# Kernel optimization log

Measured on AMD Instinct MI355X. Metric: run time of the kernel, lower is better.

The kernel has to match this reference:

```python
import jax, jax.numpy as jnp
import numpy as np

D_MODEL = 1024
NUM_HEADS = 16
DEPTH = D_MODEL // NUM_HEADS
NEG = -1e30


def setup_inputs() -> dict:
    key = jax.random.key(0)
    ks = jax.random.split(key, 12)
    B, S = 4, 2048
    scale = 1.0 / np.sqrt(D_MODEL)
    inp = {
        "v": jax.random.normal(ks[0], (B, S, D_MODEL), dtype=jnp.float32),
        "k": jax.random.normal(ks[1], (B, S, D_MODEL), dtype=jnp.float32),
        "q": jax.random.normal(ks[2], (B, S, D_MODEL), dtype=jnp.float32),
        "mask": jax.random.randint(ks[3], (B, 1, 1, S), 0, 2, dtype=jnp.int32),
        "wq": jax.random.normal(ks[4], (D_MODEL, D_MODEL), dtype=jnp.float32) * scale,
        "bq": jnp.zeros((D_MODEL,), dtype=jnp.float32),
        "wk": jax.random.normal(ks[5], (D_MODEL, D_MODEL), dtype=jnp.float32) * scale,
        "bk": jnp.zeros((D_MODEL,), dtype=jnp.float32),
        "wv": jax.random.normal(ks[6], (D_MODEL, D_MODEL), dtype=jnp.float32) * scale,
        "bv": jnp.zeros((D_MODEL,), dtype=jnp.float32),
        "wo": jax.random.normal(ks[7], (D_MODEL, D_MODEL), dtype=jnp.float32) * scale,
        "bo": jnp.zeros((D_MODEL,), dtype=jnp.float32),
    }
    return inp


def _split_heads(x):
    # [B, S, D] -> [B, H, S, depth]
    B, S, _ = x.shape
    return x.reshape(B, S, NUM_HEADS, DEPTH).transpose(0, 2, 1, 3)


def reference(v, k, q, mask, wq, bq, wk, bk, wv, bv, wo, bo):
    B, Sq, _ = q.shape
    qh = _split_heads(q @ wq + bq)  # [B,H,Sq,depth]
    kh = _split_heads(k @ wk + bk)  # [B,H,Sk,depth]
    vh = _split_heads(v @ wv + bv)  # [B,H,Sk,depth]
    scale = 1.0 / jnp.sqrt(jnp.float32(DEPTH))
    scores = scale * jnp.einsum("bhqd,bhkd->bhqk", qh, kh)
    scores = scores + mask.astype(scores.dtype) * NEG
    attn = jax.nn.softmax(scores, axis=-1)
    out = jnp.einsum("bhqk,bhkd->bhqd", attn, vh)
    out = out.transpose(0, 2, 1, 3).reshape(B, Sq, D_MODEL)
    return out @ wo + bo
```

## Files before the change

kernel.cpp:

```cpp
#include <hip/hip_runtime.h>

typedef _Float16 half_t;
typedef __attribute__((ext_vector_type(8))) _Float16 half8;
typedef __attribute__((ext_vector_type(4))) _Float16 half4;
typedef __attribute__((ext_vector_type(4))) float f32x4;

#define SEQ   2048
#define DM    1024
#define NH    16
#define DEPTH 64

__device__ __forceinline__ void gload16(const void* g, void* l) {
    __builtin_amdgcn_global_load_lds(
        (const __attribute__((address_space(1))) void*)g,
        (__attribute__((address_space(3))) void*)l, 16, 0, 0);
}

__global__ __launch_bounds__(256) void wm_k(
    const float* __restrict__ w0, const float* __restrict__ w1,
    const float* __restrict__ w2, const float* __restrict__ w3,
    half_t* __restrict__ out,
    const int* __restrict__ mask, int* __restrict__ idx, int* __restrict__ cnt)
{
    const int z = blockIdx.z;
    if (z == 4) {
        if (blockIdx.x || blockIdx.y) return;
        const int tid = threadIdx.y * 32 + threadIdx.x;
        const int b = tid >> 6;
        const int lane = tid & 63;
        const int* m = mask + b*SEQ;
        int* ib = idx + b*SEQ;
        int off = 0;
        for (int c = 0; c < SEQ; c += 64) {
            int keep = (m[c + lane] == 0);
            unsigned long long bal = __ballot(keep);
            int pre = __popcll(bal & ((1ull << lane) - 1ull));
            if (keep) ib[off + pre] = c + lane;
            off += __popcll(bal);
        }
        if (lane == 0) cnt[b] = off;
        return;
    }
    __shared__ float tile[32][33];
    const float* srcs[4] = {w0, w1, w2, w3};
    const float* src = srcs[z];
    half_t* dst = out + (size_t)z * DM * DM;
    int n0 = blockIdx.x * 32, k0 = blockIdx.y * 32;
    int tx = threadIdx.x, ty = threadIdx.y;
#pragma unroll
    for (int i = 0; i < 4; ++i)
        tile[ty + 8*i][tx] = src[(size_t)(k0 + ty + 8*i)*DM + n0 + tx];
    __syncthreads();
#pragma unroll
    for (int i = 0; i < 4; ++i)
        dst[(size_t)(n0 + ty + 8*i)*DM + k0 + tx] = (half_t)tile[tx][ty + 8*i];
}

__global__ __launch_bounds__(256) void cvt3_k(
    const float* __restrict__ qsrc, const float* __restrict__ ksrc,
    const float* __restrict__ vsrc,
    const int* __restrict__ idx, const int* __restrict__ cnt,
    half_t* __restrict__ qdst, half_t* __restrict__ kdst, half_t* __restrict__ vdst)
{
    const int bid = blockIdx.x;
    const int t = threadIdx.x;
    if (bid < 4096) {
        size_t i = ((size_t)bid * 256 + t) * 8;
        float4 a = *(const float4*)(qsrc + i);
        float4 b = *(const float4*)(qsrc + i + 4);
        half8 h;
        h[0]=(half_t)a.x; h[1]=(half_t)a.y; h[2]=(half_t)a.z; h[3]=(half_t)a.w;
        h[4]=(half_t)b.x; h[5]=(half_t)b.y; h[6]=(half_t)b.z; h[7]=(half_t)b.w;
        *(half8*)(qdst + i) = h;
        return;
    }
    const int which = (bid >= 4608);
    const float* src = which ? vsrc : ksrc;
    half_t*      dst = which ? vdst : kdst;
    const int r0 = (bid - (which ? 4608 : 4096)) * 16;
    const int b  = r0 >> 11;
    const int nc = cnt[b];
    const int row = r0 + (t >> 4);
    const int jl  = row & (SEQ - 1);
    if (jl >= nc) return;
    const float* sp = src + (size_t)((b << 11) + idx[(b << 11) + jl]) * DM;
    half_t* dp = dst + (size_t)row * DM;
#pragma unroll
    for (int i = 0; i < 8; ++i) {
        int c = i*128 + (t & 15)*8;
        float4 lo = *(const float4*)(sp + c);
        float4 hi = *(const float4*)(sp + c + 4);
        half8 h;
        h[0]=(half_t)lo.x; h[1]=(half_t)lo.y; h[2]=(half_t)lo.z; h[3]=(half_t)lo.w;
        h[4]=(half_t)hi.x; h[5]=(half_t)hi.y; h[6]=(half_t)hi.z; h[7]=(half_t)hi.w;
        *(half8*)(dp + c) = h;
    }
}

__global__ __launch_bounds__(512, 2) void qk8_k(
    const half_t* __restrict__ Aq, const half_t* __restrict__ Ak,
    const half_t* __restrict__ wT,
    const float* __restrict__ bq, const float* __restrict__ bk,
    float qscale,
    half_t* __restrict__ Qh, half_t* __restrict__ Kc)
{
    __shared__ __align__(16) half_t smem[3 * 24576];
    const int flat = blockIdx.x;
    const int wg   = (flat & 7) * 64 + (flat >> 3);
    const int z    = wg >> 8;
    const int rem  = wg & 255;
    const int n0   = (rem & 3) * 256;
    const int m0   = (rem >> 2) * 128;

    const half_t* A    = z ? Ak : Aq;
    const half_t* Bt   = wT + (size_t)z * DM * DM;
    const float*  bias = z ? bk : bq;
    half_t*       Cp   = z ? Kc : Qh;
    const float   os   = z ? 1.0f : qscale;

    const int t = threadIdx.x, lane = t & 63, wave = t >> 6;
    const int wr = wave >> 2, wc = wave & 3;
    const int lr = lane & 15, lq = lane >> 4;

    f32x4 acc[4][4] = {};

#pragma unroll
    for (int kt = 0; kt < 2; ++kt) {
#pragma unroll
        for (int i = 0; i < 2; ++i) {
            int c = i*512 + t;
            gload16(A + (size_t)(m0 + (c>>3))*DM + kt*64 + (c&7)*8,
                    smem + kt*24576 + c*8);
        }
#pragma unroll
        for (int i = 0; i < 4; ++i) {
            int c = i*512 + t;
            gload16(Bt + (size_t)(n0 + (c>>3))*DM + kt*64 + (c&7)*8,
                    smem + kt*24576 + 8192 + c*8);
        }
    }
    asm volatile("s_waitcnt vmcnt(6)" ::: "memory");
    __builtin_amdgcn_s_barrier();

    for (int kt = 0; kt < 16; ++kt) {
        const int cur = kt % 3;
        const half_t* lA = smem + cur*24576;
        const half_t* lB = smem + cur*24576 + 8192;

        half8 af[4][2], bf[4][2];
#pragma unroll
        for (int mi = 0; mi < 4; ++mi)
#pragma unroll
            for (int kk = 0; kk < 2; ++kk)
                af[mi][kk] = *(const half8*)(lA + (wr*64 + mi*16 + lr)*64 + kk*32 + lq*8);
#pragma unroll
        for (int ni = 0; ni < 4; ++ni)
#pragma unroll
            for (int kk = 0; kk < 2; ++kk)
                bf[ni][kk] = *(const half8*)(lB + (wc*64 + ni*16 + lr)*64 + kk*32 + lq*8);

        if (kt + 2 < 16) {
            const int nxt = (kt + 2) % 3;
            const int kn = kt + 2;
#pragma unroll
            for (int i = 0; i < 2; ++i) {
                int c = i*512 + t;
                gload16(A + (size_t)(m0 + (c>>3))*DM + kn*64 + (c&7)*8,
                        smem + nxt*24576 + c*8);
            }
#pragma unroll
            for (int i = 0; i < 4; ++i) {
                int c = i*512 + t;
                gload16(Bt + (size_t)(n0 + (c>>3))*DM + kn*64 + (c&7)*8,
                        smem + nxt*24576 + 8192 + c*8);
            }
        }

        __builtin_amdgcn_s_setprio(1);
#pragma unroll
        for (int mi = 0; mi < 4; ++mi)
#pragma unroll
            for (int ni = 0; ni < 4; ++ni)
#pragma unroll
                for (int kk = 0; kk < 2; ++kk)
                    acc[mi][ni] = __builtin_amdgcn_mfma_f32_16x16x32_f16(af[mi][kk], bf[ni][kk], acc[mi][ni], 0, 0, 0);
        __builtin_amdgcn_s_setprio(0);

        if (kt < 15) {
            if (kt < 14) asm volatile("s_waitcnt vmcnt(6)" ::: "memory");
            else         asm volatile("s_waitcnt vmcnt(0)" ::: "memory");
            __builtin_amdgcn_s_barrier();
        }
    }

#pragma unroll
    for (int mi = 0; mi < 4; ++mi) {
#pragma unroll
        for (int ni = 0; ni < 4; ++ni) {
            int col = n0 + wc*64 + ni*16 + lr;
            float bv = bias[col];
#pragma unroll
            for (int j = 0; j < 4; ++j) {
                int row = m0 + wr*64 + mi*16 + lq*4 + j;
                Cp[(size_t)row*DM + col] = (half_t)((acc[mi][ni][j] + bv) * os);
            }
        }
    }
}

template<bool OUT_F32, bool VEPI>
__global__ __launch_bounds__(512, 2) void proj8_f16(
    const half_t* __restrict__ A, const half_t* __restrict__ Bt,
    const float* __restrict__ bias, float oscale, void* __restrict__ Cp)
{
    __shared__ __align__(16) half_t smem[3 * 24576];
    const int flat = blockIdx.x;
    const int wg   = (flat & 7) * 32 + (flat >> 3);
    const int n0   = (wg & 3) * 256;
    const int m0   = (wg >> 2) * 128;
    const int t = threadIdx.x, lane = t & 63, wave = t >> 6;
    const int wr = wave >> 2, wc = wave & 3;
    const int lr = lane & 15, lq = lane >> 4;

    f32x4 acc[4][4] = {};

#pragma unroll
    for (int kt = 0; kt < 2; ++kt) {
#pragma unroll
        for (int i = 0; i < 2; ++i) {
            int c = i*512 + t;
            gload16(A + (size_t)(m0 + (c>>3))*DM + kt*64 + (c&7)*8,
                    smem + kt*24576 + c*8);
        }
#pragma unroll
        for (int i = 0; i < 4; ++i) {
            int c = i*512 + t;
            gload16(Bt + (size_t)(n0 + (c>>3))*DM + kt*64 + (c&7)*8,
                    smem + kt*24576 + 8192 + c*8);
        }
    }
    asm volatile("s_waitcnt vmcnt(6)" ::: "memory");
    __builtin_amdgcn_s_barrier();

    for (int kt = 0; kt < 16; ++kt) {
        const int cur = kt % 3;
        const half_t* lA = smem + cur*24576;
        const half_t* lB = smem + cur*24576 + 8192;

        half8 af[4][2], bf[4][2];
#pragma unroll
        for (int mi = 0; mi < 4; ++mi)
#pragma unroll
            for (int kk = 0; kk < 2; ++kk)
                af[mi][kk] = *(const half8*)(lA + (wr*64 + mi*16 + lr)*64 + kk*32 + lq*8);
#pragma unroll
        for (int ni = 0; ni < 4; ++ni)
#pragma unroll
            for (int kk = 0; kk < 2; ++kk)
                bf[ni][kk] = *(const half8*)(lB + (wc*64 + ni*16 + lr)*64 + kk*32 + lq*8);

        if (kt + 2 < 16) {
            const int nxt = (kt + 2) % 3;
            const int kn = kt + 2;
#pragma unroll
            for (int i = 0; i < 2; ++i) {
                int c = i*512 + t;
                gload16(A + (size_t)(m0 + (c>>3))*DM + kn*64 + (c&7)*8,
                        smem + nxt*24576 + c*8);
            }
#pragma unroll
            for (int i = 0; i < 4; ++i) {
                int c = i*512 + t;
                gload16(Bt + (size_t)(n0 + (c>>3))*DM + kn*64 + (c&7)*8,
                        smem + nxt*24576 + 8192 + c*8);
            }
        }

        __builtin_amdgcn_s_setprio(1);
#pragma unroll
        for (int mi = 0; mi < 4; ++mi)
#pragma unroll
            for (int ni = 0; ni < 4; ++ni)
#pragma unroll
                for (int kk = 0; kk < 2; ++kk)
                    acc[mi][ni] = __builtin_amdgcn_mfma_f32_16x16x32_f16(af[mi][kk], bf[ni][kk], acc[mi][ni], 0, 0, 0);
        __builtin_amdgcn_s_setprio(0);

        if (kt < 15) {
            if (kt < 14) asm volatile("s_waitcnt vmcnt(6)" ::: "memory");
            else         asm volatile("s_waitcnt vmcnt(0)" ::: "memory");
            __builtin_amdgcn_s_barrier();
        }
    }

    const int b = m0 >> 11;
#pragma unroll
    for (int mi = 0; mi < 4; ++mi) {
#pragma unroll
        for (int ni = 0; ni < 4; ++ni) {
            int col = n0 + wc*64 + ni*16 + lr;
            float bv = bias[col];
            if (VEPI) {
                int rl = (m0 + wr*64 + mi*16 + lq*4) & (SEQ-1);
                int pos = (rl & ~63) | (((rl>>5)&1)<<5) | (((rl>>2)&3)<<3) | (((rl>>4)&1)<<2);
                half4 hv;
#pragma unroll
                for (int j = 0; j < 4; ++j)
                    hv[j] = (half_t)(acc[mi][ni][j] + bv);
                *(half4*)((half_t*)Cp + ((size_t)(b*NH*DEPTH + col))*SEQ + pos) = hv;
            } else {
#pragma unroll
                for (int j = 0; j < 4; ++j) {
                    int row = m0 + wr*64 + mi*16 + lq*4 + j;
                    float vv = (acc[mi][ni][j] + bv) * oscale;
                    if (OUT_F32)
                        ((float*)Cp)[(size_t)row*DM + col] = vv;
                    else
                        ((half_t*)Cp)[(size_t)row*DM + col] = (half_t)vv;
                }
            }
        }
    }
}

__global__ __launch_bounds__(512, 4) void attn_k(
    const half_t* __restrict__ Qh, const half_t* __restrict__ Kc,
    const half_t* __restrict__ Vt, const int* __restrict__ cnt,
    half_t* __restrict__ Oh)
{
    constexpr int KP = 72;
    constexpr int VP = 136;
    __shared__ __align__(16) half_t lK[2][128 * KP];
    __shared__ __align__(16) half_t lV[2][64 * VP];
    const int t = threadIdx.x;
    const int lane = t & 63, wave = t >> 6;
    const int lr = lane & 15, lq = lane >> 4;
    const int flat = blockIdx.x;
    const int rest = flat >> 3;
    const int qb = rest & 7;
    const int bh = (flat & 7) + 8 * (rest >> 3);
    const int b = bh >> 4, h = bh & 15;
    const int q0 = qb * 256;

    const int nc = cnt[b];
    const int ntk = (nc + 127) >> 7;

    const size_t qbase = ((size_t)(b*SEQ + q0 + wave*32 + lr))*DM + h*DEPTH;
    const half8 aq00 = *(const half8*)(Qh + qbase + lq*8);
    const half8 aq01 = *(const half8*)(Qh + qbase + 32 + lq*8);
    const half8 aq10 = *(const half8*)(Qh + qbase + (size_t)16*DM + lq*8);
    const half8 aq11 = *(const half8*)(Qh + qbase + (size_t)16*DM + 32 + lq*8);

    const int krow = t >> 2, kcol = (t & 3) * 16;
    const int vd   = t >> 3, vs   = (t & 7) * 16;
    const half_t* gK = Kc + (size_t)(b*SEQ + krow)*DM + h*DEPTH + kcol;
    const half_t* gV = Vt + ((size_t)bh*DEPTH + vd)*SEQ + vs;

    f32x4 o[2][4] = {};
    f32x4 ol[2] = {};
    half8 onesv;
#pragma unroll
    for (int e = 0; e < 8; ++e) onesv[e] = (half_t)1.0f;
    const f32x4 minit = {-8.0f, -8.0f, -8.0f, -8.0f};

    half8 kr0 = *(const half8*)gK,       kr1 = *(const half8*)(gK + 8);
    half8 vr0 = *(const half8*)gV,       vr1 = *(const half8*)(gV + 8);
    *(half8*)&lK[0][krow*KP + kcol]     = kr0;
    *(half8*)&lK[0][krow*KP + kcol + 8] = kr1;
    *(half8*)&lV[0][vd*VP + vs]         = vr0;
    *(half8*)&lV[0][vd*VP + vs + 8]     = vr1;
    __syncthreads();

    for (int it = 0; it < ntk; ++it) {
        const int cur = it & 1;
        const int kt = it * 128;
        const bool more = (it + 1 < ntk);
        if (more) {
            const half_t* nk = gK + (size_t)(it+1)*128*DM;
            const half_t* nv = gV + (it+1)*128;
            kr0 = *(const half8*)nk;  kr1 = *(const half8*)(nk + 8);
            vr0 = *(const half8*)nv;  vr1 = *(const half8*)(nv + 8);
        }
        const bool full = (kt + 128 <= nc);

#pragma unroll
        for (int c = 0; c < 4; ++c) {
            f32x4 s[2][2] = {{minit, minit}, {minit, minit}};
            __builtin_amdgcn_s_setprio(1);
#pragma unroll
            for (int cc = 0; cc < 2; ++cc) {
                const half_t* kb = &lK[cur][((2*c+cc)*16 + lr)*KP];
                half8 kf0 = *(const half8*)(kb + lq*8);
                half8 kf1 = *(const half8*)(kb + 32 + lq*8);
                s[0][cc] = __builtin_amdgcn_mfma_f32_16x16x32_f16(kf0, aq00, s[0][cc], 0, 0, 0);
                s[0][cc] = __builtin_amdgcn_mfma_f32_16x16x32_f16(kf1, aq01, s[0][cc], 0, 0, 0);
                s[1][cc] = __builtin_amdgcn_mfma_f32_16x16x32_f16(kf0, aq10, s[1][cc], 0, 0, 0);
                s[1][cc] = __builtin_amdgcn_mfma_f32_16x16x32_f16(kf1, aq11, s[1][cc], 0, 0, 0);
            }
            __builtin_amdgcn_s_setprio(0);

            half8 pk0, pk1;
            if (full) {
#pragma unroll
                for (int cc = 0; cc < 2; ++cc)
#pragma unroll
                    for (int r = 0; r < 4; ++r) {
                        pk0[cc*4 + r] = (half_t)__builtin_amdgcn_exp2f(s[0][cc][r]);
                        pk1[cc*4 + r] = (half_t)__builtin_amdgcn_exp2f(s[1][cc][r]);
                    }
            } else {
#pragma unroll
                for (int cc = 0; cc < 2; ++cc)
#pragma unroll
                    for (int r = 0; r < 4; ++r) {
                        float am = (kt + (2*c+cc)*16 + lq*4 + r < nc) ? 0.0f : -1e30f;
                        pk0[cc*4 + r] = (half_t)__builtin_amdgcn_exp2f(s[0][cc][r] + am);
                        pk1[cc*4 + r] = (half_t)__builtin_amdgcn_exp2f(s[1][cc][r] + am);
                    }
            }

            __builtin_amdgcn_s_setprio(1);
#pragma unroll
            for (int ni = 0; ni < 4; ++ni) {
                half8 av = *(const half8*)(&lV[cur][(ni*16 + lr)*VP + c*32 + lq*8]);
                o[0][ni] = __builtin_amdgcn_mfma_f32_16x16x32_f16(av, pk0, o[0][ni], 0, 0, 0);
                o[1][ni] = __builtin_amdgcn_mfma_f32_16x16x32_f16(av, pk1, o[1][ni], 0, 0, 0);
            }
            ol[0] = __builtin_amdgcn_mfma_f32_16x16x32_f16(onesv, pk0, ol[0], 0, 0, 0);
            ol[1] = __builtin_amdgcn_mfma_f32_16x16x32_f16(onesv, pk1, ol[1], 0, 0, 0);
            __builtin_amdgcn_s_setprio(0);
        }

        if (more) {
            *(half8*)&lK[cur^1][krow*KP + kcol]     = kr0;
            *(half8*)&lK[cur^1][krow*KP + kcol + 8] = kr1;
            *(half8*)&lV[cur^1][vd*VP + vs]         = vr0;
            *(half8*)&lV[cur^1][vd*VP + vs + 8]     = vr1;
        }
        __syncthreads();
    }

    half_t* pb = ((half_t*)lK) + wave * 32 * KP;
    float rl0 = 1.0f / ol[0][0];
    float rl1 = 1.0f / ol[1][0];
#pragma unroll
    for (int ni = 0; ni < 4; ++ni)
#pragma unroll
        for (int j = 0; j < 4; ++j) {
            pb[lr*KP + ni*16 + lq*4 + j]        = (half_t)(o[0][ni][j] * rl0);
            pb[(16 + lr)*KP + ni*16 + lq*4 + j] = (half_t)(o[1][ni][j] * rl1);
        }
    __syncthreads();
#pragma unroll
    for (int rr = 0; rr < 4; ++rr) {
        int qq = rr*8 + (lane >> 3);
        int c = (lane & 7) * 8;
        half8 hv = *(const half8*)(pb + qq*KP + c);
        *(half8*)(Oh + (size_t)(b*SEQ + q0 + wave*32 + qq)*DM + h*DEPTH + c) = hv;
    }
}

extern "C" void kernel_launch(void* const* d_in, const int* in_sizes, int n_in,
                              void* d_out, int out_size, void* d_ws, size_t ws_size,
                              hipStream_t stream) {
    (void)in_sizes; (void)n_in; (void)out_size; (void)ws_size;
    const float* v    = (const float*)d_in[0];
    const float* k    = (const float*)d_in[1];
    const float* q    = (const float*)d_in[2];
    const int*   mask = (const int*)  d_in[3];
    const float* wq   = (const float*)d_in[4];
    const float* bq   = (const float*)d_in[5];
    const float* wk   = (const float*)d_in[6];
    const float* bk   = (const float*)d_in[7];
    const float* wv   = (const float*)d_in[8];
    const float* bv   = (const float*)d_in[9];
    const float* wo   = (const float*)d_in[10];
    const float* bo   = (const float*)d_in[11];

    half_t* wT  = (half_t*)d_ws;
    half_t* xfq = wT + 4ull*1024*1024;
    half_t* xfk = xfq + 8ull*1024*1024;
    half_t* xfv = xfk + 8ull*1024*1024;
    half_t* Kc  = xfv + 8ull*1024*1024;
    half_t* Qh  = (half_t*)d_out;
    half_t* Vt  = xfq;
    half_t* O16 = xfv;

    int* idx = (int*)((char*)d_out + 32ull*1024*1024 - 65536);
    int* cnt = idx + 4*SEQ;

    const float qscale = 0.125f * 1.44269504088896340736f;

    wm_k<<<dim3(32,32,5), dim3(32,8), 0, stream>>>(wq, wk, wv, wo, wT, mask, idx, cnt);
    cvt3_k<<<5120, 256, 0, stream>>>(q, k, v, idx, cnt, xfq, xfk, xfv);

    qk8_k<<<512, 512, 0, stream>>>(xfq, xfk, wT, bq, bk, qscale, Qh, Kc);
    proj8_f16<false,true><<<256, 512, 0, stream>>>(xfv, wT + 2ull*1024*1024, bv, 1.0f, Vt);

    attn_k<<<512, 512, 0, stream>>>(Qh, Kc, Vt, cnt, O16);
    proj8_f16<true,false><<<256, 512, 0, stream>>>(O16, wT + 3ull*1024*1024, bo, 1.0f, (float*)d_out);
}
```

Measured before the change: 187.8 us.

## Halve GEMM K-tile to 32 with XOR-swizzled LDS layout in projection kernels

Reduces the K-step of the Q/K and output projection GEMMs from 64 to 32, halving LDS per stage from 144KB to 72KB across three buffers, and doubling the number of pipeline iterations. The global-to-LDS loads now XOR-swizzle the 16-byte chunks by row group, and the fragment reads apply the matching swizzle to avoid LDS bank conflicts. The smaller footprint may allow more workgroups per CU. The cost is twice as many barriers and waitcnt points per tile, with less MFMA work between syncs.

```diff
diff --git a/kernel.cpp b/kernel.cpp
--- a/kernel.cpp
+++ b/kernel.cpp
@@ -97,6 +97,7 @@
     }
 }
 
+
 __global__ __launch_bounds__(512, 2) void qk8_k(
     const half_t* __restrict__ Aq, const half_t* __restrict__ Ak,
     const half_t* __restrict__ wT,
@@ -104,7 +105,7 @@
     float qscale,
     half_t* __restrict__ Qh, half_t* __restrict__ Kc)
 {
-    __shared__ __align__(16) half_t smem[3 * 24576];
+    __shared__ __align__(16) half_t smem[3 * 12288];
     const int flat = blockIdx.x;
     const int wg   = (flat & 7) * 64 + (flat >> 3);
     const int z    = wg >> 8;
@@ -121,58 +122,48 @@
     const int t = threadIdx.x, lane = t & 63, wave = t >> 6;
     const int wr = wave >> 2, wc = wave & 3;
     const int lr = lane & 15, lq = lane >> 4;
-
+    const int lx = (lr >> 2) & 3;
+
+    const int ar = t >> 2,  asl = t & 3;
     f32x4 acc[4][4] = {};
 
 #pragma unroll
     for (int kt = 0; kt < 2; ++kt) {
+        gload16(A + (size_t)(m0 + ar)*DM + kt*32 + ((asl ^ ((ar>>2)&3))*8),
+                smem + kt*12288 + t*8);
 #pragma unroll
         for (int i = 0; i < 2; ++i) {
-            int c = i*512 + t;
-            gload16(A + (size_t)(m0 + (c>>3))*DM + kt*64 + (c&7)*8,
-                    smem + kt*24576 + c*8);
-        }
-#pragma unroll
-        for (int i = 0; i < 4; ++i) {
-            int c = i*512 + t;
-            gload16(Bt + (size_t)(n0 + (c>>3))*DM + kt*64 + (c&7)*8,
-                    smem + kt*24576 + 8192 + c*8);
-        }
-    }
-    asm volatile("s_waitcnt vmcnt(6)" ::: "memory");
+            int c = i*512 + t, r = c>>2, s = c&3;
+            gload16(Bt + (size_t)(n0 + r)*DM + kt*32 + ((s ^ ((r>>2)&3))*8),
+                    smem + kt*12288 + 4096 + c*8);
+        }
+    }
+    asm volatile("s_waitcnt vmcnt(3)" ::: "memory");
     __builtin_amdgcn_s_barrier();
 
-    for (int kt = 0; kt < 16; ++kt) {
+    for (int kt = 0; kt < 32; ++kt) {
         const int cur = kt % 3;
-        const half_t* lA = smem + cur*24576;
-        const half_t* lB = smem + cur*24576 + 8192;
-
-        half8 af[4][2], bf[4][2];
+        const half_t* lA = smem + cur*12288;
+        const half_t* lB = smem + cur*12288 + 4096;
+
+        half8 af[4], bf[4];
 #pragma unroll
         for (int mi = 0; mi < 4; ++mi)
-#pragma unroll
-            for (int kk = 0; kk < 2; ++kk)
-                af[mi][kk] = *(const half8*)(lA + (wr*64 + mi*16 + lr)*64 + kk*32 + lq*8);
+            af[mi] = *(const half8*)(lA + (wr*64 + mi*16 + lr)*32 + ((lq ^ lx))*8);
 #pragma unroll
         for (int ni = 0; ni < 4; ++ni)
-#pragma unroll
-            for (int kk = 0; kk < 2; ++kk)
-                bf[ni][kk] = *(const half8*)(lB + (wc*64 + ni*16 + lr)*64 + kk*32 + lq*8);
-
-        if (kt + 2 < 16) {
+            bf[ni] = *(const half8*)(lB + (wc*64 + ni*16 + lr)*32 + ((lq ^ lx))*8);
+
+        if (kt + 2 < 32) {
             const int nxt = (kt + 2) % 3;
             const int kn = kt + 2;
+            gload16(A + (size_t)(m0 + ar)*DM + kn*32 + ((asl ^ ((ar>>2)&3))*8),
+                    smem + nxt*12288 + t*8);
 #pragma unroll
             for (int i = 0; i < 2; ++i) {
-                int c = i*512 + t;
-                gload16(A + (size_t)(m0 + (c>>3))*DM + kn*64 + (c&7)*8,
-                        smem + nxt*24576 + c*8);
-            }
-#pragma unroll
-            for (int i = 0; i < 4; ++i) {
-                int c = i*512 + t;
-                gload16(Bt + (size_t)(n0 + (c>>3))*DM + kn*64 + (c&7)*8,
-                        smem + nxt*24576 + 8192 + c*8);
+                int c = i*512 + t, r = c>>2, s = c&3;
+                gload16(Bt + (size_t)(n0 + r)*DM + kn*32 + ((s ^ ((r>>2)&3))*8),
+                        smem + nxt*12288 + 4096 + c*8);
             }
         }
 
@@ -181,13 +172,11 @@
         for (int mi = 0; mi < 4; ++mi)
 #pragma unroll
             for (int ni = 0; ni < 4; ++ni)
-#pragma unroll
-                for (int kk = 0; kk < 2; ++kk)
-                    acc[mi][ni] = __builtin_amdgcn_mfma_f32_16x16x32_f16(af[mi][kk], bf[ni][kk], acc[mi][ni], 0, 0, 0);
+                acc[mi][ni] = __builtin_amdgcn_mfma_f32_16x16x32_f16(af[mi], bf[ni], acc[mi][ni], 0, 0, 0);
         __builtin_amdgcn_s_setprio(0);
 
-        if (kt < 15) {
-            if (kt < 14) asm volatile("s_waitcnt vmcnt(6)" ::: "memory");
+        if (kt < 31) {
+            if (kt < 30) asm volatile("s_waitcnt vmcnt(3)" ::: "memory");
             else         asm volatile("s_waitcnt vmcnt(0)" ::: "memory");
             __builtin_amdgcn_s_barrier();
         }
@@ -213,7 +202,7 @@
     const half_t* __restrict__ A, const half_t* __restrict__ Bt,
     const float* __restrict__ bias, float oscale, void* __restrict__ Cp)
 {
-    __shared__ __align__(16) half_t smem[3 * 24576];
+    __shared__ __align__(16) half_t smem[3 * 12288];
     const int flat = blockIdx.x;
     const int wg   = (flat & 7) * 32 + (flat >> 3);
     const int n0   = (wg & 3) * 256;
@@ -221,58 +210,48 @@
     const int t = threadIdx.x, lane = t & 63, wave = t >> 6;
     const int wr = wave >> 2, wc = wave & 3;
     const int lr = lane & 15, lq = lane >> 4;
+    const int lx = (lr >> 2) & 3;
+    const int ar = t >> 2,  asl = t & 3;
 
     f32x4 acc[4][4] = {};
 
 #pragma unroll
     for (int kt = 0; kt < 2; ++kt) {
+        gload16(A + (size_t)(m0 + ar)*DM + kt*32 + ((asl ^ ((ar>>2)&3))*8),
+                smem + kt*12288 + t*8);
 #pragma unroll
         for (int i = 0; i < 2; ++i) {
-            int c = i*512 + t;
-            gload16(A + (size_t)(m0 + (c>>3))*DM + kt*64 + (c&7)*8,
-                    smem + kt*24576 + c*8);
-        }
-#pragma unroll
-        for (int i = 0; i < 4; ++i) {
-            int c = i*512 + t;
-            gload16(Bt + (size_t)(n0 + (c>>3))*DM + kt*64 + (c&7)*8,
-                    smem + kt*24576 + 8192 + c*8);
-        }
-    }
-    asm volatile("s_waitcnt vmcnt(6)" ::: "memory");
+            int c = i*512 + t, r = c>>2, s = c&3;
+            gload16(Bt + (size_t)(n0 + r)*DM + kt*32 + ((s ^ ((r>>2)&3))*8),
+                    smem + kt*12288 + 4096 + c*8);
+        }
+    }
+    asm volatile("s_waitcnt vmcnt(3)" ::: "memory");
     __builtin_amdgcn_s_barrier();
 
-    for (int kt = 0; kt < 16; ++kt) {
+    for (int kt = 0; kt < 32; ++kt) {
         const int cur = kt % 3;
-        const half_t* lA = smem + cur*24576;
-        const half_t* lB = smem + cur*24576 + 8192;
-
-        half8 af[4][2], bf[4][2];
+        const half_t* lA = smem + cur*12288;
+        const half_t* lB = smem + cur*12288 + 4096;
+
+        half8 af[4], bf[4];
 #pragma unroll
         for (int mi = 0; mi < 4; ++mi)
-#pragma unroll
-            for (int kk = 0; kk < 2; ++kk)
-                af[mi][kk] = *(const half8*)(lA + (wr*64 + mi*16 + lr)*64 + kk*32 + lq*8);
+            af[mi] = *(const half8*)(lA + (wr*64 + mi*16 + lr)*32 + ((lq ^ lx))*8);
 #pragma unroll
         for (int ni = 0; ni < 4; ++ni)
-#pragma unroll
-            for (int kk = 0; kk < 2; ++kk)
-                bf[ni][kk] = *(const half8*)(lB + (wc*64 + ni*16 + lr)*64 + kk*32 + lq*8);
-
-        if (kt + 2 < 16) {
+            bf[ni] = *(const half8*)(lB + (wc*64 + ni*16 + lr)*32 + ((lq ^ lx))*8);
+
+        if (kt + 2 < 32) {
             const int nxt = (kt + 2) % 3;
             const int kn = kt + 2;
+            gload16(A + (size_t)(m0 + ar)*DM + kn*32 + ((asl ^ ((ar>>2)&3))*8),
+                    smem + nxt*12288 + t*8);
 #pragma unroll
             for (int i = 0; i < 2; ++i) {
-                int c = i*512 + t;
-                gload16(A + (size_t)(m0 + (c>>3))*DM + kn*64 + (c&7)*8,
-                        smem + nxt*24576 + c*8);
-            }
-#pragma unroll
-            for (int i = 0; i < 4; ++i) {
-                int c = i*512 + t;
-                gload16(Bt + (size_t)(n0 + (c>>3))*DM + kn*64 + (c&7)*8,
-                        smem + nxt*24576 + 8192 + c*8);
+                int c = i*512 + t, r = c>>2, s = c&3;
+                gload16(Bt + (size_t)(n0 + r)*DM + kn*32 + ((s ^ ((r>>2)&3))*8),
+                        smem + nxt*12288 + 4096 + c*8);
             }
         }
 
@@ -281,13 +260,11 @@
         for (int mi = 0; mi < 4; ++mi)
 #pragma unroll
             for (int ni = 0; ni < 4; ++ni)
-#pragma unroll
-                for (int kk = 0; kk < 2; ++kk)
-                    acc[mi][ni] = __builtin_amdgcn_mfma_f32_16x16x32_f16(af[mi][kk], bf[ni][kk], acc[mi][ni], 0, 0, 0);
+                acc[mi][ni] = __builtin_amdgcn_mfma_f32_16x16x32_f16(af[mi], bf[ni], acc[mi][ni], 0, 0, 0);
         __builtin_amdgcn_s_setprio(0);
 
-        if (kt < 15) {
-            if (kt < 14) asm volatile("s_waitcnt vmcnt(6)" ::: "memory");
+        if (kt < 31) {
+            if (kt < 30) asm volatile("s_waitcnt vmcnt(3)" ::: "memory");
             else         asm volatile("s_waitcnt vmcnt(0)" ::: "memory");
             __builtin_amdgcn_s_barrier();
         }
```

Result: faster. 179.3 us (-4.5%).
